# Kernel tuning notes

Measured on AMD Instinct MI355X. Metric: run time of the kernel, lower is better.

The kernel has to match this reference:

```python
import jax, jax.numpy as jnp
import numpy as np

DIM = 1024
N_HEADS = 16
HEAD_DIM = DIM // N_HEADS
B, T = 4, 2048


def setup_inputs() -> dict:
    key = jax.random.key(0)
    k_x, k_cos, k_sin, k_wqkv, k_wout = jax.random.split(key, 5)
    x = jax.random.normal(k_x, (B, T, DIM), dtype=jnp.float32)
    # rotary tables indexed by position, half the head dim
    pos = jnp.arange(T, dtype=jnp.float32)[:, None]
    inv_freq = 1.0 / (10000.0 ** (jnp.arange(0, HEAD_DIM, 2, dtype=jnp.float32) / HEAD_DIM))
    ang = pos * inv_freq[None, :]  # [T, HEAD_DIM//2]
    cos = jnp.cos(ang)
    sin = jnp.sin(ang)
    mask = jnp.zeros((T, T), dtype=jnp.float32)
    Wqkv = jax.random.normal(k_wqkv, (3 * DIM, DIM), dtype=jnp.float32) * 0.02
    Wout = jax.random.normal(k_wout, (DIM, DIM), dtype=jnp.float32) * 0.02
    return {"x": x, "cos": cos, "sin": sin, "mask": mask, "Wqkv": Wqkv, "Wout": Wout}


def _apply_rope(t, cos, sin):
    # t: [B, T, H, D]; cos/sin: [T, D//2]
    d = t.shape[-1]
    t1, t2 = t[..., : d // 2], t[..., d // 2 :]
    c = cos[: t.shape[1]][None, :, None, :]
    s = sin[: t.shape[1]][None, :, None, :]
    return jnp.concatenate([t1 * c - t2 * s, t1 * s + t2 * c], axis=-1)


def reference(x, cos, sin, mask, Wqkv, Wout):
    Bx, Tx, C = x.shape
    scale = HEAD_DIM ** -0.5
    qkv = (x @ Wqkv.T).reshape(Bx, Tx, 3, N_HEADS, HEAD_DIM)
    q, k, v = qkv[:, :, 0], qkv[:, :, 1], qkv[:, :, 2]
    q = _apply_rope(q, cos, sin)
    k = _apply_rope(k, cos, sin)
    attn = jnp.einsum("bthd,bshd->bhts", q, k) * scale  # [B, H, T, T]
    attn = attn + mask[None, None, :, :]
    p = jax.nn.softmax(attn, axis=-1)
    out = jnp.einsum("bhts,bshd->bthd", p, v).reshape(Bx, Tx, C)
    return out @ Wout.T
```

## Files before the change

kernel.cpp:

```cpp
#include <hip/hip_runtime.h>
#include <math.h>

#define DIMC   1024
#define NHEADS 16
#define HD     64
#define BATCH  4
#define SEQ    2048
#define MROWS  (BATCH * SEQ)
#define QKVC   (3 * DIMC)
#define QSCALE 0.1803368801111204f

typedef __bf16 bf16x8 __attribute__((ext_vector_type(8)));
typedef float  f32x4  __attribute__((ext_vector_type(4)));
typedef unsigned short us;

#define MFMA16(a, b, c) __builtin_amdgcn_mfma_f32_16x16x32_bf16(a, b, c, 0, 0, 0)

__device__ __forceinline__ void async16(const void* g, void* l) {
    __builtin_amdgcn_global_load_lds(
        (const __attribute__((address_space(1))) void*)g,
        (__attribute__((address_space(3))) void*)l, 16, 0, 0);
}

__device__ __forceinline__ bf16x8 ldsfrag(const us* p) {
    union { int4 q; bf16x8 v; } u;
    u.q = *(const int4*)p;
    return u.v;
}

__device__ __forceinline__ bf16x8 gfrag(const us* __restrict__ p) {
    union { int4 q; bf16x8 v; } u;
    u.q = *(const int4*)p;
    return u.v;
}

__device__ __forceinline__ us bf16_rn(float f) {
    unsigned int u = __builtin_bit_cast(unsigned int, f);
    u += 0x7fffu + ((u >> 16) & 1u);
    return (us)(u >> 16);
}

__device__ __forceinline__ float fast_exp2(float x) {
#if __has_builtin(__builtin_amdgcn_exp2f)
    return __builtin_amdgcn_exp2f(x);
#else
    return __expf(x * 0.6931471805599453f);
#endif
}

__device__ __forceinline__ bf16x8 pack8t(const float* p) {
    union { unsigned int u[4]; bf16x8 v; } z;
#pragma unroll
    for (int i = 0; i < 4; ++i) {
        unsigned int lo = __builtin_bit_cast(unsigned int, p[2 * i]);
        unsigned int hi = __builtin_bit_cast(unsigned int, p[2 * i + 1]);
        z.u[i] = __builtin_amdgcn_perm(hi, lo, 0x07060302);
    }
    return z.v;
}

#define NX (MROWS * DIMC)
#define NW (QKVC * DIMC)
#define NO (DIMC * DIMC)
__global__ __launch_bounds__(256) void cast3_bf16(const float* __restrict__ x,
                                                  const float* __restrict__ wq,
                                                  const float* __restrict__ wo,
                                                  us* __restrict__ xb,
                                                  us* __restrict__ wqb,
                                                  us* __restrict__ wob) {
    int i = (blockIdx.x * 256 + threadIdx.x) * 4;
    const float* src;
    us* dst;
    if (i < NX)               { src = x  + i;            dst = xb  + i; }
    else if (i < NX + NW)     { src = wq + (i - NX);     dst = wqb + (i - NX); }
    else if (i < NX + NW + NO){ src = wo + (i - NX - NW);dst = wob + (i - NX - NW); }
    else return;
    float4 v = *(const float4*)src;
    ushort4 o = {bf16_rn(v.x), bf16_rn(v.y), bf16_rn(v.z), bf16_rn(v.w)};
    *(ushort4*)dst = o;
}

template <int MODE>
__global__ __launch_bounds__(256) void gemm_bt(const us* __restrict__ A,
                                               const us* __restrict__ B,
                                               void* __restrict__ Cv,
                                               const float* __restrict__ cosb,
                                               const float* __restrict__ sinb,
                                               int M, int N, int K) {
    __shared__ __align__(16) us As[128 * 32];
    __shared__ __align__(16) us Bs[128 * 32];

    const int tid  = threadIdx.x;
    const int lane = tid & 63, w = tid >> 6;
    const int col  = lane & 15, quad = lane >> 4;
    const int m0   = blockIdx.y * 128, n0 = blockIdx.x * 128;
    const int wm   = (w >> 1) * 64,   wn = (w & 1) * 64;

    const int srow = w * 32 + (lane >> 2);
    const int scol = (lane & 3) * 8;
    const us* Ag = A + (size_t)(m0 + srow) * K + scol;
    const us* Bg = B + (size_t)(n0 + srow) * K + scol;
    us* Asl = As + w * 1024 + lane * 8;
    us* Bsl = Bs + w * 1024 + lane * 8;

    f32x4 acc[4][4] = {};

    for (int k0 = 0; k0 < K; k0 += 32) {
        __syncthreads();
        async16(Ag + k0, Asl);
        async16(Ag + (size_t)16 * K + k0, Asl + 512);
        async16(Bg + k0, Bsl);
        async16(Bg + (size_t)16 * K + k0, Bsl + 512);
        __syncthreads();

        bf16x8 af[4], bfr[4];
#pragma unroll
        for (int mt = 0; mt < 4; ++mt)
            af[mt] = ldsfrag(As + (wm + mt * 16 + col) * 32 + quad * 8);
#pragma unroll
        for (int nt = 0; nt < 4; ++nt)
            bfr[nt] = ldsfrag(Bs + (wn + nt * 16 + col) * 32 + quad * 8);
#pragma unroll
        for (int mt = 0; mt < 4; ++mt)
#pragma unroll
            for (int nt = 0; nt < 4; ++nt)
                acc[mt][nt] = MFMA16(af[mt], bfr[nt], acc[mt][nt]);
    }

    if constexpr (MODE == 1) {
        us* C = (us*)Cv;
        const int gcol0 = n0 + wn;
        const bool is_v = (gcol0 >= 2 * DIMC);
        const float f = (gcol0 < DIMC) ? QSCALE : 1.0f;
#pragma unroll
        for (int mt = 0; mt < 4; ++mt) {
#pragma unroll
            for (int r = 0; r < 4; ++r) {
                const int grow = m0 + wm + mt * 16 + quad * 4 + r;
                if (is_v) {
#pragma unroll
                    for (int nt = 0; nt < 4; ++nt)
                        C[(size_t)grow * N + gcol0 + nt * 16 + col] =
                            bf16_rn(acc[mt][nt][r]);
                } else {
                    const int t = grow & (SEQ - 1);
#pragma unroll
                    for (int nt = 0; nt < 2; ++nt) {
                        const int d1 = nt * 16 + col;
                        const float c = cosb[t * 32 + d1];
                        const float s = sinb[t * 32 + d1];
                        const float v1 = acc[mt][nt][r];
                        const float v2 = acc[mt][nt + 2][r];
                        C[(size_t)grow * N + gcol0 + d1]      = bf16_rn((v1 * c - v2 * s) * f);
                        C[(size_t)grow * N + gcol0 + d1 + 32] = bf16_rn((v1 * s + v2 * c) * f);
                    }
                }
            }
        }
    } else {
        float* C = (float*)Cv;
#pragma unroll
        for (int mt = 0; mt < 4; ++mt)
#pragma unroll
            for (int nt = 0; nt < 4; ++nt)
#pragma unroll
                for (int r = 0; r < 4; ++r)
                    C[(size_t)(m0 + wm + mt * 16 + quad * 4 + r) * N +
                      n0 + wn + nt * 16 + col] = acc[mt][nt][r];
    }
}

__global__ __launch_bounds__(256) void transpose_v(const us* __restrict__ qkv,
                                                   us* __restrict__ vt) {
    __shared__ us L[64][66];
    const int tid = threadIdx.x;
    const int bh = blockIdx.y, b = bh >> 4, h = bh & 15;
    const int t0 = blockIdx.x * 64;

    {
        const int tr = tid >> 2, dc = (tid & 3) * 16;
        const us* src = qkv + (size_t)(b * SEQ + t0 + tr) * QKVC + 2 * DIMC + h * HD + dc;
        *(int4*)&L[tr][dc]     = *(const int4*)src;
        *(int4*)&L[tr][dc + 8] = *(const int4*)(src + 8);
    }
    __syncthreads();
    {
        const int d = tid >> 2, tc = (tid & 3) * 16;
        unsigned int wb[8];
#pragma unroll
        for (int i = 0; i < 8; ++i)
            wb[i] = (unsigned int)L[tc + 2 * i][d] |
                    ((unsigned int)L[tc + 2 * i + 1][d] << 16);
        us* dst = vt + ((size_t)bh * HD + d) * SEQ + t0 + tc;
        *(int4*)dst       = make_int4(wb[0], wb[1], wb[2], wb[3]);
        *(int4*)(dst + 8) = make_int4(wb[4], wb[5], wb[6], wb[7]);
    }
}

__global__ __launch_bounds__(256, 2) void attn_mfma(const us* __restrict__ qkv,
                                                    const us* __restrict__ vt,
                                                    us* __restrict__ outb) {
    __shared__ __align__(16) us Ks[64 * 64];
    __shared__ __align__(16) us Vs[64 * 64];
    __shared__ __align__(16) float Ps[4][16 * 68];

    const int tid  = threadIdx.x;
    const int lane = tid & 63, w = tid >> 6;
    const int col  = lane & 15, quad = lane >> 4;
    const int bh = blockIdx.y, b = bh >> 4, h = bh & 15;
    const int t0 = blockIdx.x * 256;

    const int r8 = lane >> 3;
    const int cs = ((lane & 7) ^ r8) * 8;

    const int sw0 = ((quad ^ (col & 7)) << 3);
    const int sw4 = sw0 ^ 32;

    const us* qb = qkv + (size_t)b * SEQ * QKVC + h * HD;

    bf16x8 aq[4][2];
#pragma unroll
    for (int s = 0; s < 4; ++s)
#pragma unroll
        for (int hf = 0; hf < 2; ++hf)
            aq[s][hf] = gfrag(qb + (size_t)(t0 + s * 64 + w * 16 + col) * QKVC +
                              hf * 32 + quad * 8);

    const us* kg0 = qkv + (size_t)(b * SEQ + w * 16 + r8) * QKVC + DIMC + h * HD + cs;
    const us* vg0 = vt + ((size_t)bh * HD + w * 16 + r8) * SEQ + cs;
    us* kl = Ks + w * 1024 + lane * 8;
    us* vl = Vs + w * 1024 + lane * 8;

    union { us u[8]; bf16x8 v; } ones;
#pragma unroll
    for (int i = 0; i < 8; ++i) ones.u[i] = 0x3F80;

    f32x4 o_acc[4][4] = {};
    f32x4 lacc[4] = {};
    float* Pw = &Ps[w][0];

    for (int s0 = 0; s0 < SEQ; s0 += 64) {
        __syncthreads();
        async16(kg0 + (size_t)s0 * QKVC, kl);
        async16(kg0 + (size_t)(s0 + 8) * QKVC, kl + 512);
        async16(vg0 + s0, vl);
        async16(vg0 + s0 + (size_t)8 * SEQ, vl + 512);
        __syncthreads();

        bf16x8 bk[4][2], bv[4][2];
#pragma unroll
        for (int nt = 0; nt < 4; ++nt) {
            bk[nt][0] = ldsfrag(Ks + (nt * 16 + col) * 64 + sw0);
            bk[nt][1] = ldsfrag(Ks + (nt * 16 + col) * 64 + sw4);
            bv[nt][0] = ldsfrag(Vs + (nt * 16 + col) * 64 + sw0);
            bv[nt][1] = ldsfrag(Vs + (nt * 16 + col) * 64 + sw4);
        }

#pragma unroll
        for (int s = 0; s < 4; ++s) {
            f32x4 sacc[4] = {};
#pragma unroll
            for (int nt = 0; nt < 4; ++nt) {
                sacc[nt] = MFMA16(aq[s][0], bk[nt][0], sacc[nt]);
                sacc[nt] = MFMA16(aq[s][1], bk[nt][1], sacc[nt]);
            }
#pragma unroll
            for (int nt = 0; nt < 4; ++nt)
#pragma unroll
                for (int r = 0; r < 4; ++r)
                    Pw[(quad * 4 + r) * 68 + nt * 16 + col] = fast_exp2(sacc[nt][r]);

#pragma unroll
            for (int ks = 0; ks < 2; ++ks) {
                bf16x8 ap = pack8t(Pw + col * 68 + ks * 32 + quad * 8);
                lacc[s] = MFMA16(ap, ones.v, lacc[s]);
#pragma unroll
                for (int nt = 0; nt < 4; ++nt)
                    o_acc[s][nt] = MFMA16(ap, bv[nt][ks], o_acc[s][nt]);
            }
        }
    }

#pragma unroll
    for (int s = 0; s < 4; ++s) {
        float linv[4];
#pragma unroll
        for (int r = 0; r < 4; ++r) linv[r] = __builtin_amdgcn_rcpf(lacc[s][r]);
#pragma unroll
        for (int nt = 0; nt < 4; ++nt)
#pragma unroll
            for (int r = 0; r < 4; ++r) {
                const int t = t0 + s * 64 + w * 16 + quad * 4 + r;
                const int d = h * HD + nt * 16 + col;
                outb[(size_t)(b * SEQ + t) * DIMC + d] = bf16_rn(o_acc[s][nt][r] * linv[r]);
            }
    }
}

extern "C" void kernel_launch(void* const* d_in, const int* in_sizes, int n_in,
                              void* d_out, int out_size, void* d_ws, size_t ws_size,
                              hipStream_t stream) {
    const float* x    = (const float*)d_in[0];
    const float* cosb = (const float*)d_in[1];
    const float* sinb = (const float*)d_in[2];
    const float* Wqkv = (const float*)d_in[4];
    const float* Wout = (const float*)d_in[5];
    float* out = (float*)d_out;

    us* xb    = (us*)d_ws;
    us* wqkb  = xb + (size_t)MROWS * DIMC;
    us* woutb = wqkb + (size_t)QKVC * DIMC;
    us* qkvb  = woutb + (size_t)DIMC * DIMC;
    us* vtb   = qkvb + (size_t)MROWS * QKVC;
    us* aob   = vtb + (size_t)BATCH * NHEADS * HD * SEQ;

    cast3_bf16<<<(NX + NW + NO) / 1024, 256, 0, stream>>>(x, Wqkv, Wout,
                                                          xb, wqkb, woutb);

    gemm_bt<1><<<dim3(QKVC / 128, MROWS / 128), 256, 0, stream>>>(
        xb, wqkb, qkvb, cosb, sinb, MROWS, QKVC, DIMC);

    transpose_v<<<dim3(SEQ / 64, BATCH * NHEADS), 256, 0, stream>>>(qkvb, vtb);

    attn_mfma<<<dim3(SEQ / 256, BATCH * NHEADS), 256, 0, stream>>>(qkvb, vtb, aob);

    gemm_bt<0><<<dim3(DIMC / 128, MROWS / 128), 256, 0, stream>>>(
        aob, woutb, out, nullptr, nullptr, MROWS, DIMC, DIMC);
}
```

Baseline: 319.6 us.

## Keep softmax probabilities in registers via transposed QK^T and 16x16x16 MFMA

The attention kernel now computes S transposed (K as the A operand), so each lane's exp2 results already sit in the layout of a 16x16x16 bf16 MFMA A-operand. This removes the per-wave LDS scratch buffer for P and the store/reload round trip. V fragments are read as 64-bit LDS loads to match, and the PV product and row-sum use twice as many smaller MFMAs. Separately, cos and sin are interleaved into one float2 table in the cast kernel so the QKV GEMM epilogue issues one load per position instead of two. The interleaved table costs extra workspace.

```diff
diff --git a/kernel.cpp b/kernel.cpp
--- a/kernel.cpp
+++ b/kernel.cpp
@@ -12,9 +12,20 @@
 
 typedef __bf16 bf16x8 __attribute__((ext_vector_type(8)));
 typedef float  f32x4  __attribute__((ext_vector_type(4)));
+typedef short  s16x4  __attribute__((ext_vector_type(4)));
 typedef unsigned short us;
 
 #define MFMA16(a, b, c) __builtin_amdgcn_mfma_f32_16x16x32_bf16(a, b, c, 0, 0, 0)
+
+__device__ __forceinline__ f32x4 mfma16x16x16(s16x4 a, s16x4 b, f32x4 c) {
+#if __has_builtin(__builtin_amdgcn_mfma_f32_16x16x16bf16_1k)
+    return __builtin_amdgcn_mfma_f32_16x16x16bf16_1k(a, b, c, 0, 0, 0);
+#else
+    asm volatile("v_mfma_f32_16x16x16_bf16 %0, %1, %2, %0"
+                 : "+v"(c) : "v"(a), "v"(b));
+    return c;
+#endif
+}
 
 __device__ __forceinline__ void async16(const void* g, void* l) {
     __builtin_amdgcn_global_load_lds(
@@ -25,6 +36,12 @@
 __device__ __forceinline__ bf16x8 ldsfrag(const us* p) {
     union { int4 q; bf16x8 v; } u;
     u.q = *(const int4*)p;
+    return u.v;
+}
+
+__device__ __forceinline__ s16x4 ldsfrag64(const us* p) {
+    union { uint2 q; s16x4 v; } u;
+    u.q = *(const uint2*)p;
     return u.v;
 }
 
@@ -48,33 +65,45 @@
 #endif
 }
 
-__device__ __forceinline__ bf16x8 pack8t(const float* p) {
-    union { unsigned int u[4]; bf16x8 v; } z;
-#pragma unroll
-    for (int i = 0; i < 4; ++i) {
-        unsigned int lo = __builtin_bit_cast(unsigned int, p[2 * i]);
-        unsigned int hi = __builtin_bit_cast(unsigned int, p[2 * i + 1]);
-        z.u[i] = __builtin_amdgcn_perm(hi, lo, 0x07060302);
-    }
+__device__ __forceinline__ s16x4 pack4t(float a, float b, float c, float d) {
+    union { unsigned u[2]; s16x4 v; } z;
+    z.u[0] = __builtin_amdgcn_perm(__builtin_bit_cast(unsigned, b),
+                                   __builtin_bit_cast(unsigned, a), 0x07060302);
+    z.u[1] = __builtin_amdgcn_perm(__builtin_bit_cast(unsigned, d),
+                                   __builtin_bit_cast(unsigned, c), 0x07060302);
     return z.v;
 }
 
 #define NX (MROWS * DIMC)
 #define NW (QKVC * DIMC)
 #define NO (DIMC * DIMC)
+#define NC (SEQ * 32)
 __global__ __launch_bounds__(256) void cast3_bf16(const float* __restrict__ x,
                                                   const float* __restrict__ wq,
                                                   const float* __restrict__ wo,
+                                                  const float* __restrict__ cosb,
+                                                  const float* __restrict__ sinb,
                                                   us* __restrict__ xb,
                                                   us* __restrict__ wqb,
-                                                  us* __restrict__ wob) {
+                                                  us* __restrict__ wob,
+                                                  float* __restrict__ cs2) {
     int i = (blockIdx.x * 256 + threadIdx.x) * 4;
     const float* src;
     us* dst;
-    if (i < NX)               { src = x  + i;            dst = xb  + i; }
-    else if (i < NX + NW)     { src = wq + (i - NX);     dst = wqb + (i - NX); }
-    else if (i < NX + NW + NO){ src = wo + (i - NX - NW);dst = wob + (i - NX - NW); }
-    else return;
+    if (i < NX)                { src = x  + i;             dst = xb  + i; }
+    else if (i < NX + NW)      { src = wq + (i - NX);      dst = wqb + (i - NX); }
+    else if (i < NX + NW + NO) { src = wo + (i - NX - NW); dst = wob + (i - NX - NW); }
+    else {
+        int p0 = i - (NX + NW + NO);
+        if (p0 >= NC) return;
+        float4 c4 = *(const float4*)(cosb + p0);
+        float4 s4 = *(const float4*)(sinb + p0);
+        float4 o0 = {c4.x, s4.x, c4.y, s4.y};
+        float4 o1 = {c4.z, s4.z, c4.w, s4.w};
+        *(float4*)(cs2 + 2 * p0)     = o0;
+        *(float4*)(cs2 + 2 * p0 + 4) = o1;
+        return;
+    }
     float4 v = *(const float4*)src;
     ushort4 o = {bf16_rn(v.x), bf16_rn(v.y), bf16_rn(v.z), bf16_rn(v.w)};
     *(ushort4*)dst = o;
@@ -84,8 +113,7 @@
 __global__ __launch_bounds__(256) void gemm_bt(const us* __restrict__ A,
                                                const us* __restrict__ B,
                                                void* __restrict__ Cv,
-                                               const float* __restrict__ cosb,
-                                               const float* __restrict__ sinb,
+                                               const float* __restrict__ cs2,
                                                int M, int N, int K) {
     __shared__ __align__(16) us As[128 * 32];
     __shared__ __align__(16) us Bs[128 * 32];
@@ -147,12 +175,11 @@
 #pragma unroll
                     for (int nt = 0; nt < 2; ++nt) {
                         const int d1 = nt * 16 + col;
-                        const float c = cosb[t * 32 + d1];
-                        const float s = sinb[t * 32 + d1];
+                        const float2 cs = ((const float2*)cs2)[t * 32 + d1];
                         const float v1 = acc[mt][nt][r];
                         const float v2 = acc[mt][nt + 2][r];
-                        C[(size_t)grow * N + gcol0 + d1]      = bf16_rn((v1 * c - v2 * s) * f);
-                        C[(size_t)grow * N + gcol0 + d1 + 32] = bf16_rn((v1 * s + v2 * c) * f);
+                        C[(size_t)grow * N + gcol0 + d1]      = bf16_rn((v1 * cs.x - v2 * cs.y) * f);
+                        C[(size_t)grow * N + gcol0 + d1 + 32] = bf16_rn((v1 * cs.y + v2 * cs.x) * f);
                     }
                 }
             }
@@ -202,7 +229,6 @@
                                                     us* __restrict__ outb) {
     __shared__ __align__(16) us Ks[64 * 64];
     __shared__ __align__(16) us Vs[64 * 64];
-    __shared__ __align__(16) float Ps[4][16 * 68];
 
     const int tid  = threadIdx.x;
     const int lane = tid & 63, w = tid >> 6;
@@ -215,6 +241,7 @@
 
     const int sw0 = ((quad ^ (col & 7)) << 3);
     const int sw4 = sw0 ^ 32;
+    const int e2 = quad >> 1, o4 = (quad & 1) * 4, cm = col & 7;
 
     const us* qb = qkv + (size_t)b * SEQ * QKVC + h * HD;
 
@@ -231,13 +258,12 @@
     us* kl = Ks + w * 1024 + lane * 8;
     us* vl = Vs + w * 1024 + lane * 8;
 
-    union { us u[8]; bf16x8 v; } ones;
-#pragma unroll
-    for (int i = 0; i < 8; ++i) ones.u[i] = 0x3F80;
+    union { us u[4]; s16x4 v; } ones4;
+#pragma unroll
+    for (int i = 0; i < 4; ++i) ones4.u[i] = 0x3F80;
 
     f32x4 o_acc[4][4] = {};
     f32x4 lacc[4] = {};
-    float* Pw = &Ps[w][0];
 
     for (int s0 = 0; s0 < SEQ; s0 += 64) {
         __syncthreads();
@@ -247,37 +273,39 @@
         async16(vg0 + s0 + (size_t)8 * SEQ, vl + 512);
         __syncthreads();
 
-        bf16x8 bk[4][2], bv[4][2];
+        bf16x8 bk[4][2];
+        s16x4  bv[4][4];
 #pragma unroll
         for (int nt = 0; nt < 4; ++nt) {
             bk[nt][0] = ldsfrag(Ks + (nt * 16 + col) * 64 + sw0);
             bk[nt][1] = ldsfrag(Ks + (nt * 16 + col) * 64 + sw4);
-            bv[nt][0] = ldsfrag(Vs + (nt * 16 + col) * 64 + sw0);
-            bv[nt][1] = ldsfrag(Vs + (nt * 16 + col) * 64 + sw4);
+#pragma unroll
+            for (int dt = 0; dt < 4; ++dt)
+                bv[nt][dt] = ldsfrag64(Vs + (dt * 16 + col) * 64 +
+                                       (((nt * 2 + e2) ^ cm) << 3) + o4);
         }
 
 #pragma unroll
         for (int s = 0; s < 4; ++s) {
-            f32x4 sacc[4] = {};
+            f32x4 st[4] = {};
 #pragma unroll
             for (int nt = 0; nt < 4; ++nt) {
-                sacc[nt] = MFMA16(aq[s][0], bk[nt][0], sacc[nt]);
-                sacc[nt] = MFMA16(aq[s][1], bk[nt][1], sacc[nt]);
+                st[nt] = MFMA16(bk[nt][0], aq[s][0], st[nt]);
+                st[nt] = MFMA16(bk[nt][1], aq[s][1], st[nt]);
             }
+            s16x4 ap[4];
 #pragma unroll
             for (int nt = 0; nt < 4; ++nt)
-#pragma unroll
-                for (int r = 0; r < 4; ++r)
-                    Pw[(quad * 4 + r) * 68 + nt * 16 + col] = fast_exp2(sacc[nt][r]);
-
-#pragma unroll
-            for (int ks = 0; ks < 2; ++ks) {
-                bf16x8 ap = pack8t(Pw + col * 68 + ks * 32 + quad * 8);
-                lacc[s] = MFMA16(ap, ones.v, lacc[s]);
+                ap[nt] = pack4t(fast_exp2(st[nt][0]), fast_exp2(st[nt][1]),
+                                fast_exp2(st[nt][2]), fast_exp2(st[nt][3]));
+#pragma unroll
+            for (int nt = 0; nt < 4; ++nt)
+                lacc[s] = mfma16x16x16(ap[nt], ones4.v, lacc[s]);
+#pragma unroll
+            for (int dt = 0; dt < 4; ++dt)
 #pragma unroll
                 for (int nt = 0; nt < 4; ++nt)
-                    o_acc[s][nt] = MFMA16(ap, bv[nt][ks], o_acc[s][nt]);
-            }
+                    o_acc[s][dt] = mfma16x16x16(ap[nt], bv[nt][dt], o_acc[s][dt]);
         }
     }
 
@@ -287,12 +315,12 @@
 #pragma unroll
         for (int r = 0; r < 4; ++r) linv[r] = __builtin_amdgcn_rcpf(lacc[s][r]);
 #pragma unroll
-        for (int nt = 0; nt < 4; ++nt)
+        for (int dt = 0; dt < 4; ++dt)
 #pragma unroll
             for (int r = 0; r < 4; ++r) {
                 const int t = t0 + s * 64 + w * 16 + quad * 4 + r;
-                const int d = h * HD + nt * 16 + col;
-                outb[(size_t)(b * SEQ + t) * DIMC + d] = bf16_rn(o_acc[s][nt][r] * linv[r]);
+                const int d = h * HD + dt * 16 + col;
+                outb[(size_t)(b * SEQ + t) * DIMC + d] = bf16_rn(o_acc[s][dt][r] * linv[r]);
             }
     }
 }
@@ -313,17 +341,18 @@
     us* qkvb  = woutb + (size_t)DIMC * DIMC;
     us* vtb   = qkvb + (size_t)MROWS * QKVC;
     us* aob   = vtb + (size_t)BATCH * NHEADS * HD * SEQ;
-
-    cast3_bf16<<<(NX + NW + NO) / 1024, 256, 0, stream>>>(x, Wqkv, Wout,
-                                                          xb, wqkb, woutb);
+    float* cs2 = (float*)(aob + (size_t)MROWS * DIMC);
+
+    cast3_bf16<<<(NX + NW + NO + NC) / 1024, 256, 0, stream>>>(
+        x, Wqkv, Wout, cosb, sinb, xb, wqkb, woutb, cs2);
 
     gemm_bt<1><<<dim3(QKVC / 128, MROWS / 128), 256, 0, stream>>>(
-        xb, wqkb, qkvb, cosb, sinb, MROWS, QKVC, DIMC);
+        xb, wqkb, qkvb, cs2, MROWS, QKVC, DIMC);
 
     transpose_v<<<dim3(SEQ / 64, BATCH * NHEADS), 256, 0, stream>>>(qkvb, vtb);
 
     attn_mfma<<<dim3(SEQ / 256, BATCH * NHEADS), 256, 0, stream>>>(qkvb, vtb, aob);
 
     gemm_bt<0><<<dim3(DIMC / 128, MROWS / 128), 256, 0, stream>>>(
-        aob, woutb, out, nullptr, nullptr, MROWS, DIMC, DIMC);
-}
+        aob, woutb, out, nullptr, MROWS, DIMC, DIMC);
+}
```

Result: faster. 310.5 us (-2.8%).
